# Kernel optimization log

Measured on AMD Instinct MI355X. Metric: run time of the kernel, lower is better.

Reference implementation:

```python
import jax, jax.numpy as jnp
import numpy as np


def setup_inputs() -> dict:
    key = jax.random.key(0)
    k1, k2, k3 = jax.random.split(key, 3)
    B, T, F = 16, 8192, 512
    x = jax.random.normal(k1, (B, T, F), dtype=jnp.float32)
    initial_state = jax.random.normal(k2, (B, F), dtype=jnp.float32)
    # learned smoothing coefficient, shape [1], initialized near coeff_init=0.04
    smooth = jnp.full((1,), 0.04, dtype=jnp.float32)
    return {"x": x, "initial_state": initial_state, "smooth": smooth}


def reference(x, initial_state, smooth):
    # x: [B, T, F], initial_state: [B, F], smooth: [1]
    w = jnp.clip(smooth, 0.0, 1.0)  # [1], broadcasts over [B, F]
    xt = jnp.transpose(x, (1, 0, 2))  # time-major [T, B, F]

    def step(a, xi):
        a = w * xi + (1.0 - w) * a
        return a, a

    _, ys = jax.lax.scan(step, initial_state, xt)  # ys: [T, B, F]
    return jnp.transpose(ys, (1, 0, 2))  # [B, T, F]
```

## Files before the change

### kernel.cpp

```cpp
#include <hip/hip_runtime.h>
#include <hip/hip_bf16.h>

#define B_   16
#define T_   8192
#define F_   512
#define F4_  (F_ / 4)
#define BF4_ (B_ * F4_)

typedef float f4v __attribute__((ext_vector_type(4)));

__device__ __forceinline__ float read_w(const float* smooth) {
    float w = smooth[0];
    return fminf(fmaxf(w, 0.0f), 1.0f);
}

__global__ __launch_bounds__(256, 4) void ema_phase1(const float* __restrict__ x,
                                                     const float* __restrict__ smooth,
                                                     float4* __restrict__ carry,
                                                     int C, int L) {
    const int tid = blockIdx.x * blockDim.x + threadIdx.x;
    const int lc  = 31 - __clz(C);
    const int f4  = tid & (F4_ - 1);
    const int c   = (tid >> 7) & (C - 1);
    const int b   = tid >> (7 + lc);
    const float w = read_w(smooth);
    const float d = 1.0f - w;

    const float4* xp = reinterpret_cast<const float4*>(x)
                     + (size_t)(b * T_ + c * L) * F4_ + f4;
    float4 a = make_float4(0.f, 0.f, 0.f, 0.f);
#pragma unroll 8
    for (int s = 0; s < L; ++s) {
        float4 xv = xp[(size_t)s * F4_];
        a.x = fmaf(d, a.x, w * xv.x);
        a.y = fmaf(d, a.y, w * xv.y);
        a.z = fmaf(d, a.z, w * xv.z);
        a.w = fmaf(d, a.w, w * xv.w);
    }
    carry[(size_t)c * BF4_ + b * F4_ + f4] = a;
}

__global__ __launch_bounds__(256) void ema_phase2(const float* __restrict__ init,
                                                  const float* __restrict__ smooth,
                                                  float4* __restrict__ carry,
                                                  int C, int L) {
    __shared__ float4 S[256];
    const float w  = read_w(smooth);
    const float d  = 1.0f - w;
    const float dL = powf(d, (float)L);

    const int lc       = 31 - __clz(C);
    const int c        = threadIdx.x & (C - 1);
    const int colLocal = threadIdx.x >> lc;
    const int col      = blockIdx.x * (256 >> lc) + colLocal;

    float4 t = carry[(size_t)c * BF4_ + col];
    S[threadIdx.x] = t;

    float mk = dL;
    for (int step = 1; step < C; step <<= 1) {
        __syncthreads();
        float4 add = make_float4(0.f, 0.f, 0.f, 0.f);
        if (c >= step) add = S[threadIdx.x - step];
        __syncthreads();
        t.x = fmaf(mk, add.x, t.x);
        t.y = fmaf(mk, add.y, t.y);
        t.z = fmaf(mk, add.z, t.z);
        t.w = fmaf(mk, add.w, t.w);
        S[threadIdx.x] = t;
        mk *= mk;
    }
    __syncthreads();
    float4 A = make_float4(0.f, 0.f, 0.f, 0.f);
    if (c > 0) A = S[threadIdx.x - 1];
    const float4 A0 = reinterpret_cast<const float4*>(init)[col];
    const float dc = powf(dL, (float)c);
    A.x = fmaf(dc, A0.x, A.x);
    A.y = fmaf(dc, A0.y, A.y);
    A.z = fmaf(dc, A0.z, A.z);
    A.w = fmaf(dc, A0.w, A.w);
    carry[(size_t)c * BF4_ + col] = A;
}

__global__ __launch_bounds__(256, 4) void ema_phase3(const float* __restrict__ x,
                                                     const float* __restrict__ smooth,
                                                     const float4* __restrict__ carry,
                                                     float* __restrict__ y,
                                                     int C, int L) {
    const int tid = blockIdx.x * blockDim.x + threadIdx.x;
    const int lc  = 31 - __clz(C);
    const int f4  = tid & (F4_ - 1);
    const int m   = (B_ * C - 1) - (tid >> 7);
    const int c   = m & (C - 1);
    const int b   = m >> lc;
    const float w = read_w(smooth);
    const float d = 1.0f - w;

    const size_t base = (size_t)(b * T_ + c * L) * F4_ + f4;
    const f4v* xp = reinterpret_cast<const f4v*>(x) + base;
    f4v*       yp = reinterpret_cast<f4v*>(y) + base;

    float4 a = carry[(size_t)c * BF4_ + b * F4_ + f4];
#pragma unroll 8
    for (int s = 0; s < L; ++s) {
        f4v xv = __builtin_nontemporal_load(&xp[(size_t)s * F4_]);
        a.x = fmaf(d, a.x, w * xv.x);
        a.y = fmaf(d, a.y, w * xv.y);
        a.z = fmaf(d, a.z, w * xv.z);
        a.w = fmaf(d, a.w, w * xv.w);
        f4v out;
        out.x = a.x; out.y = a.y; out.z = a.z; out.w = a.w;
        __builtin_nontemporal_store(out, &yp[(size_t)s * F4_]);
    }
}

extern "C" void kernel_launch(void* const* d_in, const int* in_sizes, int n_in,
                              void* d_out, int out_size, void* d_ws, size_t ws_size,
                              hipStream_t stream) {
    const float* x      = (const float*)d_in[0];
    const float* init   = (const float*)d_in[1];
    const float* smooth = (const float*)d_in[2];
    float*       y      = (float*)d_out;
    float4*      carry  = (float4*)d_ws;

    int C = 128;
    while (C > 1 && (size_t)C * BF4_ * sizeof(float4) > ws_size) C >>= 1;
    const int L = T_ / C;

    const int threads13 = B_ * C * F4_;
    const int cpb       = 256 / C;
    ema_phase1<<<threads13 / 256, 256, 0, stream>>>(x, smooth, carry, C, L);
    ema_phase2<<<BF4_ / cpb,      256, 0, stream>>>(init, smooth, carry, C, L);
    ema_phase3<<<threads13 / 256, 256, 0, stream>>>(x, smooth, carry, y, C, L);
}
```

Baseline: 486.4 us.

## Fuse three EMA scan phases into one cooperative kernel with grid sync

Merges the chunk-carry pass, the cross-chunk prefix pass and the output pass into a single cooperative kernel separated by a grid-wide barrier. The carry buffer moves to a static device array. The log-step shared-memory scan is replaced by a per-thread serial recurrence over all preceding chunk carries. This removes two kernel launches and the inter-kernel gaps. In exchange, each thread reads up to 127 carry entries before it starts writing output, which creates load imbalance across chunks. The cooperative launch also needs all 1024 blocks to be resident at once. The reversed block order that phase 3 used for cache reuse is dropped.

```diff
diff --git a/kernel.cpp b/kernel.cpp
--- a/kernel.cpp
+++ b/kernel.cpp
@@ -1,116 +1,72 @@
 #include <hip/hip_runtime.h>
-#include <hip/hip_bf16.h>
+#include <hip/hip_cooperative_groups.h>
 
 #define B_   16
 #define T_   8192
 #define F_   512
 #define F4_  (F_ / 4)
 #define BF4_ (B_ * F4_)
+#define C_   128
+#define LC_  7
+#define L_   (T_ / C_)
 
 typedef float f4v __attribute__((ext_vector_type(4)));
 
-__device__ __forceinline__ float read_w(const float* smooth) {
+__device__ f4v g_carry[C_ * BF4_];
+
+namespace cg = cooperative_groups;
+
+__global__ __launch_bounds__(256, 4) void ema_fused(const float* __restrict__ x,
+                                                    const float* __restrict__ init,
+                                                    const float* __restrict__ smooth,
+                                                    float* __restrict__ y) {
+    const int tid = blockIdx.x * blockDim.x + threadIdx.x;
+    const int f4  = tid & (F4_ - 1);
+    const int m   = tid >> 7;
+    const int c   = m & (C_ - 1);
+    const int b   = m >> LC_;
     float w = smooth[0];
-    return fminf(fmaxf(w, 0.0f), 1.0f);
-}
-
-__global__ __launch_bounds__(256, 4) void ema_phase1(const float* __restrict__ x,
-                                                     const float* __restrict__ smooth,
-                                                     float4* __restrict__ carry,
-                                                     int C, int L) {
-    const int tid = blockIdx.x * blockDim.x + threadIdx.x;
-    const int lc  = 31 - __clz(C);
-    const int f4  = tid & (F4_ - 1);
-    const int c   = (tid >> 7) & (C - 1);
-    const int b   = tid >> (7 + lc);
-    const float w = read_w(smooth);
+    w = fminf(fmaxf(w, 0.0f), 1.0f);
     const float d = 1.0f - w;
 
-    const float4* xp = reinterpret_cast<const float4*>(x)
-                     + (size_t)(b * T_ + c * L) * F4_ + f4;
-    float4 a = make_float4(0.f, 0.f, 0.f, 0.f);
+    const size_t base = (size_t)(b * T_ + c * L_) * F4_ + f4;
+    const f4v*   xp   = reinterpret_cast<const f4v*>(x) + base;
+    const int    col  = b * F4_ + f4;
+
+    f4v a;
+    a.x = 0.f; a.y = 0.f; a.z = 0.f; a.w = 0.f;
 #pragma unroll 8
-    for (int s = 0; s < L; ++s) {
-        float4 xv = xp[(size_t)s * F4_];
+    for (int s = 0; s < L_; ++s) {
+        f4v xv = xp[(size_t)s * F4_];
         a.x = fmaf(d, a.x, w * xv.x);
         a.y = fmaf(d, a.y, w * xv.y);
         a.z = fmaf(d, a.z, w * xv.z);
         a.w = fmaf(d, a.w, w * xv.w);
     }
-    carry[(size_t)c * BF4_ + b * F4_ + f4] = a;
-}
+    g_carry[(size_t)c * BF4_ + col] = a;
 
-__global__ __launch_bounds__(256) void ema_phase2(const float* __restrict__ init,
-                                                  const float* __restrict__ smooth,
-                                                  float4* __restrict__ carry,
-                                                  int C, int L) {
-    __shared__ float4 S[256];
-    const float w  = read_w(smooth);
-    const float d  = 1.0f - w;
-    const float dL = powf(d, (float)L);
+    cg::this_grid().sync();
 
-    const int lc       = 31 - __clz(C);
-    const int c        = threadIdx.x & (C - 1);
-    const int colLocal = threadIdx.x >> lc;
-    const int col      = blockIdx.x * (256 >> lc) + colLocal;
+    const float dL = powf(d, (float)L_);
+    f4v A = reinterpret_cast<const f4v*>(init)[col];
+#pragma unroll 4
+    for (int j = 0; j < c; ++j) {
+        f4v P = g_carry[(size_t)j * BF4_ + col];
+        A.x = fmaf(dL, A.x, P.x);
+        A.y = fmaf(dL, A.y, P.y);
+        A.z = fmaf(dL, A.z, P.z);
+        A.w = fmaf(dL, A.w, P.w);
+    }
 
-    float4 t = carry[(size_t)c * BF4_ + col];
-    S[threadIdx.x] = t;
-
-    float mk = dL;
-    for (int step = 1; step < C; step <<= 1) {
-        __syncthreads();
-        float4 add = make_float4(0.f, 0.f, 0.f, 0.f);
-        if (c >= step) add = S[threadIdx.x - step];
-        __syncthreads();
-        t.x = fmaf(mk, add.x, t.x);
-        t.y = fmaf(mk, add.y, t.y);
-        t.z = fmaf(mk, add.z, t.z);
-        t.w = fmaf(mk, add.w, t.w);
-        S[threadIdx.x] = t;
-        mk *= mk;
-    }
-    __syncthreads();
-    float4 A = make_float4(0.f, 0.f, 0.f, 0.f);
-    if (c > 0) A = S[threadIdx.x - 1];
-    const float4 A0 = reinterpret_cast<const float4*>(init)[col];
-    const float dc = powf(dL, (float)c);
-    A.x = fmaf(dc, A0.x, A.x);
-    A.y = fmaf(dc, A0.y, A.y);
-    A.z = fmaf(dc, A0.z, A.z);
-    A.w = fmaf(dc, A0.w, A.w);
-    carry[(size_t)c * BF4_ + col] = A;
-}
-
-__global__ __launch_bounds__(256, 4) void ema_phase3(const float* __restrict__ x,
-                                                     const float* __restrict__ smooth,
-                                                     const float4* __restrict__ carry,
-                                                     float* __restrict__ y,
-                                                     int C, int L) {
-    const int tid = blockIdx.x * blockDim.x + threadIdx.x;
-    const int lc  = 31 - __clz(C);
-    const int f4  = tid & (F4_ - 1);
-    const int m   = (B_ * C - 1) - (tid >> 7);
-    const int c   = m & (C - 1);
-    const int b   = m >> lc;
-    const float w = read_w(smooth);
-    const float d = 1.0f - w;
-
-    const size_t base = (size_t)(b * T_ + c * L) * F4_ + f4;
-    const f4v* xp = reinterpret_cast<const f4v*>(x) + base;
-    f4v*       yp = reinterpret_cast<f4v*>(y) + base;
-
-    float4 a = carry[(size_t)c * BF4_ + b * F4_ + f4];
+    f4v* yp = reinterpret_cast<f4v*>(y) + base;
 #pragma unroll 8
-    for (int s = 0; s < L; ++s) {
+    for (int s = 0; s < L_; ++s) {
         f4v xv = __builtin_nontemporal_load(&xp[(size_t)s * F4_]);
-        a.x = fmaf(d, a.x, w * xv.x);
-        a.y = fmaf(d, a.y, w * xv.y);
-        a.z = fmaf(d, a.z, w * xv.z);
-        a.w = fmaf(d, a.w, w * xv.w);
-        f4v out;
-        out.x = a.x; out.y = a.y; out.z = a.z; out.w = a.w;
-        __builtin_nontemporal_store(out, &yp[(size_t)s * F4_]);
+        A.x = fmaf(d, A.x, w * xv.x);
+        A.y = fmaf(d, A.y, w * xv.y);
+        A.z = fmaf(d, A.z, w * xv.z);
+        A.w = fmaf(d, A.w, w * xv.w);
+        __builtin_nontemporal_store(A, &yp[(size_t)s * F4_]);
     }
 }
 
@@ -121,15 +77,10 @@
     const float* init   = (const float*)d_in[1];
     const float* smooth = (const float*)d_in[2];
     float*       y      = (float*)d_out;
-    float4*      carry  = (float4*)d_ws;
+    (void)d_ws; (void)ws_size;
 
-    int C = 128;
-    while (C > 1 && (size_t)C * BF4_ * sizeof(float4) > ws_size) C >>= 1;
-    const int L = T_ / C;
-
-    const int threads13 = B_ * C * F4_;
-    const int cpb       = 256 / C;
-    ema_phase1<<<threads13 / 256, 256, 0, stream>>>(x, smooth, carry, C, L);
-    ema_phase2<<<BF4_ / cpb,      256, 0, stream>>>(init, smooth, carry, C, L);
-    ema_phase3<<<threads13 / 256, 256, 0, stream>>>(x, smooth, carry, y, C, L);
+    void* args[] = { (void*)&x, (void*)&init, (void*)&smooth, (void*)&y };
+    const int grid = (B_ * C_ * F4_) / 256;
+    hipLaunchCooperativeKernel((const void*)ema_fused, dim3(grid), dim3(256),
+                               args, 0, stream);
 }
```

Result: slower. 608.9 us (+25.2%).
